# Optimization experiments

Measured on AMD Instinct MI355X. Metric: run time of the kernel, lower is better.

The kernel has to match this reference:

```python
import jax, jax.numpy as jnp
import numpy as np

N_NODES = 100000
N_REL = 4
N_EDGES = 160000  # per relation
IN_F, HID_F, OUT_F = 128, 128, 64


def hetero_layer(x, edges, W, b):
    """Sum over relations of GraphConv (norm='both'): D_in^-1/2 A_r D_out^-1/2 X W_r + b_r."""
    N = x.shape[0]
    out = jnp.zeros((N, W.shape[2]), dtype=x.dtype)
    for r in range(W.shape[0]):  # small fixed relation count
        src = edges[r, 0]
        dst = edges[r, 1]
        ones = jnp.ones(src.shape[0], dtype=x.dtype)
        deg_out = jnp.clip(jax.ops.segment_sum(ones, src, num_segments=N), 1.0)
        deg_in = jnp.clip(jax.ops.segment_sum(ones, dst, num_segments=N), 1.0)
        # scale src features, project (W first since in_feats >= out_feats), gather, scatter-sum
        h = (x * jax.lax.rsqrt(deg_out)[:, None]) @ W[r]
        agg = jax.ops.segment_sum(h[src], dst, num_segments=N)
        out = out + agg * jax.lax.rsqrt(deg_in)[:, None] + b[r]
    return out


def setup_inputs() -> dict:
    key = jax.random.key(0)
    ks = jax.random.split(key, 6)
    x = jax.random.normal(ks[0], (N_NODES, IN_F), dtype=jnp.float32)
    edges = jax.random.randint(ks[1], (N_REL, 2, N_EDGES), 0, N_NODES, dtype=jnp.int32)
    W1 = jax.random.normal(ks[2], (N_REL, IN_F, HID_F), dtype=jnp.float32) * 0.05
    b1 = jnp.zeros((N_REL, HID_F), dtype=jnp.float32)
    W2 = jax.random.normal(ks[3], (N_REL, HID_F, OUT_F), dtype=jnp.float32) * 0.05
    b2 = jnp.zeros((N_REL, OUT_F), dtype=jnp.float32)
    return {"x": x, "edges": edges, "W1": W1, "b1": b1, "W2": W2, "b2": b2}


def reference(x, edges, W1, b1, W2, b2):
    h = jax.nn.relu(hetero_layer(x, edges, W1, b1))
    return hetero_layer(h, edges, W2, b2)
```

## Files before the change

kernel.cpp:

```cpp
#include <hip/hip_runtime.h>
#include <cstddef>
#include <cstdint>

#define NN   100000
#define NR   4
#define NE   160000
#define SCAN_B 1024
#define GEMMB 512

typedef short bf16x8 __attribute__((ext_vector_type(8)));
typedef float f32x4  __attribute__((ext_vector_type(4)));

__device__ __forceinline__ unsigned short f2bf(float f) {
  union { float f; unsigned u; } v; v.f = f;
  unsigned r = v.u + 0x7fffu + ((v.u >> 16) & 1u);
  return (unsigned short)(r >> 16);
}
__device__ __forceinline__ float bf2f(unsigned short h) {
  union { unsigned u; float f; } v; v.u = ((unsigned)h) << 16;
  return v.f;
}

__device__ __forceinline__ void gll16(const unsigned short* g, unsigned short* l) {
  __builtin_amdgcn_global_load_lds(
      (const __attribute__((address_space(1))) void*)g,
      (__attribute__((address_space(3))) void*)l, 16, 0, 0);
}

#define A_ZERO 782
#define A_NBLK (A_ZERO + 6250 + 256 + 128 + 1)
__global__ __launch_bounds__(256) void phaseA_k(const float* __restrict__ x,
                                                const float* __restrict__ W1,
                                                const float* __restrict__ W2,
                                                const float* __restrict__ b1,
                                                const float* __restrict__ b2,
                                                int* __restrict__ cnt,
                                                unsigned short* __restrict__ xb,
                                                unsigned short* __restrict__ Wt1,
                                                unsigned short* __restrict__ Wt2,
                                                float* __restrict__ bs1,
                                                float* __restrict__ bs2) {
  const int bid = blockIdx.x;
  const int t = threadIdx.x;
  if (bid < A_ZERO) {
    const int i = bid * 256 + t;
    if (i < 2 * NR * NN / 4) ((int4*)cnt)[i] = make_int4(0, 0, 0, 0);
  } else if (bid < A_ZERO + 6250) {
    const int i = (bid - A_ZERO) * 256 + t;
    const float4 a = *(const float4*)&x[(size_t)i * 8];
    const float4 b = *(const float4*)&x[(size_t)i * 8 + 4];
    unsigned short o[8];
    o[0] = f2bf(a.x); o[1] = f2bf(a.y); o[2] = f2bf(a.z); o[3] = f2bf(a.w);
    o[4] = f2bf(b.x); o[5] = f2bf(b.y); o[6] = f2bf(b.z); o[7] = f2bf(b.w);
    *(bf16x8*)&xb[(size_t)i * 8] = *(bf16x8*)o;
  } else if (bid < A_ZERO + 6250 + 256) {
    const int i = (bid - A_ZERO - 6250) * 256 + t;
    const int r = i / (128 * 128);
    const int k = (i / 128) % 128;
    const int n = i % 128;
    Wt1[((size_t)r * 128 + n) * 128 + k] = f2bf(W1[i]);
  } else if (bid < A_ZERO + 6250 + 256 + 128) {
    const int i = (bid - A_ZERO - 6250 - 256) * 256 + t;
    const int r = i / (128 * 64);
    const int k = (i / 64) % 128;
    const int n = i % 64;
    Wt2[((size_t)r * 64 + n) * 128 + k] = f2bf(W2[i]);
  } else {
    if (t < 128) bs1[t] = b1[t] + b1[128 + t] + b1[256 + t] + b1[384 + t];
    if (t < 64)  bs2[t] = b2[t] + b2[64 + t] + b2[128 + t] + b2[192 + t];
  }
}

template <int NOUT>
__device__ __forceinline__ void gemm_core(const unsigned short* __restrict__ Xb,
                                          const unsigned short* __restrict__ Wtr,
                                          unsigned short* __restrict__ Hr,
                                          int vb, unsigned short (*Xl)[64 * 128]) {
  const int t = threadIdx.x;
  const int wid = t >> 6;
  const int lane = t & 63;
  const int lg = lane >> 4;
  const int lr = lane & 15;

  constexpr int NF = (NOUT == 128) ? 4 : 2;
  const int rbase = (wid & 1) * 32;
  const int cbase = (wid >> 1) * (NOUT / 2);

  bf16x8 bw[NF][4];
#pragma unroll
  for (int nf = 0; nf < NF; ++nf)
#pragma unroll
    for (int ks = 0; ks < 4; ++ks)
      bw[nf][ks] = *(const bf16x8*)&Wtr[(size_t)(cbase + nf * 16 + lr) * 128 + ks * 32 + lg * 8];

  auto stage = [&](int buf, int tile) {
    const int row0 = tile * 64;
#pragma unroll
    for (int i = 0; i < 4; ++i) {
      const int rl = wid * 16 + i * 4 + (lane >> 4);
      int gr = row0 + rl;
      if (gr >= NN) gr = NN - 1;
      const int q = (lane & 15) ^ (rl & 7);
      gll16(&Xb[(size_t)gr * 128 + q * 8], &Xl[buf][rl * 128 + (lane & 15) * 8]);
    }
  };

  const int ntiles = (NN + 63) / 64;
  int tile = vb;
  stage(0, tile);
  __syncthreads();
  int buf = 0;

  for (; tile < ntiles; tile += 128) {
    const int nxt = tile + 128;
    if (nxt < ntiles) stage(buf ^ 1, nxt);

    f32x4 acc[2][NF];
#pragma unroll
    for (int mf = 0; mf < 2; ++mf)
#pragma unroll
      for (int nf = 0; nf < NF; ++nf) acc[mf][nf] = (f32x4){0.f, 0.f, 0.f, 0.f};

#pragma unroll
    for (int ks = 0; ks < 4; ++ks) {
#pragma unroll
      for (int mf = 0; mf < 2; ++mf) {
        const int r = rbase + mf * 16 + lr;
        const bf16x8 a =
            *(const bf16x8*)&Xl[buf][r * 128 + (((ks * 4 + lg) ^ (lr & 7)) << 3)];
#pragma unroll
        for (int nf = 0; nf < NF; ++nf)
          acc[mf][nf] = __builtin_amdgcn_mfma_f32_16x16x32_bf16(a, bw[nf][ks], acc[mf][nf], 0, 0, 0);
      }
    }

    const int row0 = tile * 64;
#pragma unroll
    for (int mf = 0; mf < 2; ++mf) {
#pragma unroll
      for (int i = 0; i < 4; ++i) {
        const int row = row0 + rbase + mf * 16 + lg * 4 + i;
        if (row < NN) {
#pragma unroll
          for (int nf = 0; nf < NF; ++nf)
            Hr[(size_t)row * NOUT + cbase + nf * 16 + lr] = f2bf(acc[mf][nf][i]);
        }
      }
    }
    __syncthreads();
    buf ^= 1;
  }
}

__global__ __launch_bounds__(256, 2) void phaseB_k(const int* __restrict__ edges,
                                                   const unsigned short* __restrict__ xb,
                                                   const unsigned short* __restrict__ Wt1,
                                                   unsigned short* __restrict__ H,
                                                   int* __restrict__ cnt_out,
                                                   int* __restrict__ cnt_in) {
  __shared__ unsigned short Xl[2][64 * 128];
  const int bid = blockIdx.x;
  if (bid < GEMMB) {
    const int z = bid >> 7;
    gemm_core<128>(xb, Wt1 + (size_t)z * 128 * 128, H + (size_t)z * NN * 128, bid & 127, Xl);
    return;
  }
  const int idx = bid - GEMMB;
  const int r = idx / 625;
  const int e = (idx - r * 625) * 256 + threadIdx.x;
  const int s = edges[(size_t)r * 2 * NE + e];
  const int d = edges[(size_t)r * 2 * NE + NE + e];
  atomicAdd(&cnt_out[(size_t)r * NN + s], 1);
  atomicAdd(&cnt_in[(size_t)r * NN + d], 1);
}

template <int NOUT>
__global__ __launch_bounds__(256, 2) void gemm3_k(const unsigned short* __restrict__ Xb,
                                                  const unsigned short* __restrict__ Wt,
                                                  unsigned short* __restrict__ H) {
  __shared__ unsigned short Xl[2][64 * 128];
  const int z = blockIdx.z;
  gemm_core<NOUT>(Xb, Wt + (size_t)z * NOUT * 128, H + (size_t)z * NN * NOUT, blockIdx.x, Xl);
}

__global__ __launch_bounds__(256) void scan1_k(const int* __restrict__ cnt_in,
                                               int* __restrict__ excl,
                                               int* __restrict__ bsum) {
  const int b = blockIdx.x, t = threadIdx.x;
  const int base = b * SCAN_B;
  int v[4]; int tl = 0;
#pragma unroll
  for (int i = 0; i < 4; ++i) {
    const int idx = base + t * 4 + i;
    int c = 0;
    if (idx < NN) {
      c = cnt_in[idx] + cnt_in[NN + idx] + cnt_in[2 * NN + idx] + cnt_in[3 * NN + idx];
    }
    v[i] = c;
    tl += c;
  }
  __shared__ int sm[256];
  sm[t] = tl;
  __syncthreads();
  for (int off = 1; off < 256; off <<= 1) {
    const int x = (t >= off) ? sm[t - off] : 0;
    __syncthreads();
    sm[t] += x;
    __syncthreads();
  }
  const int incl = sm[t];
  int run = incl - tl;
#pragma unroll
  for (int i = 0; i < 4; ++i) {
    const int idx = base + t * 4 + i;
    if (idx < NN) excl[idx] = run;
    run += v[i];
  }
  if (t == 255) bsum[b] = incl;
}

__global__ __launch_bounds__(128) void scan2_k(int* __restrict__ bsum, int nb) {
  const int t = threadIdx.x;
  __shared__ int sm[128];
  const int v = (t < nb) ? bsum[t] : 0;
  sm[t] = v;
  __syncthreads();
  for (int off = 1; off < 128; off <<= 1) {
    const int x = (t >= off) ? sm[t - off] : 0;
    __syncthreads();
    sm[t] += x;
    __syncthreads();
  }
  if (t < nb) bsum[t] = sm[t] - v;
}

__global__ __launch_bounds__(256) void scan3rs_k(const int* __restrict__ cnt,
                                                 float* __restrict__ rs,
                                                 const int* __restrict__ bsum,
                                                 int* __restrict__ row_ptr,
                                                 int* __restrict__ cursor) {
  const int bid = blockIdx.x, t = threadIdx.x;
  if (bid < 3125) {
    const int i = bid * 256 + t;
    rs[i] = rsqrtf(fmaxf((float)cnt[i], 1.0f));
  } else {
    const int i = (bid - 3125) * 256 + t;
    if (i < NN) {
      const int v = cursor[i] + bsum[i / SCAN_B];
      row_ptr[i] = v;
      cursor[i] = v;
    }
    if (i == 0) row_ptr[NN] = NR * NE;
  }
}

__global__ __launch_bounds__(256) void fill_k(const int* __restrict__ edges,
                                              const float* __restrict__ rs_out,
                                              const float* __restrict__ rs_in,
                                              int* __restrict__ cursor,
                                              int2* __restrict__ csr) {
  const int r = blockIdx.y;
  const int e = blockIdx.x * 256 + threadIdx.x;
  if (e >= NE) return;
  const int s = edges[(size_t)r * 2 * NE + e];
  const int d = edges[(size_t)r * 2 * NE + NE + e];
  const int pos = atomicAdd(&cursor[d], 1);
  const float w = rs_in[(size_t)r * NN + d] * rs_out[(size_t)r * NN + s];
  csr[pos] = make_int2(r * NN + s, __float_as_int(w));
}

__global__ __launch_bounds__(256) void gather1_k(const unsigned short* __restrict__ H,
                                                 const int* __restrict__ row_ptr,
                                                 const int2* __restrict__ csr,
                                                 const float* __restrict__ bs1,
                                                 unsigned short* __restrict__ h1b) {
  const int node = blockIdx.x * 4 + (threadIdx.x >> 6);
  const int lane = threadIdx.x & 63;
  if (node >= NN) return;
  const int g  = lane >> 4;
  const int fl = lane & 15;

  float acc[8];
#pragma unroll
  for (int j = 0; j < 8; ++j) acc[j] = 0.f;

  const int beg = row_ptr[node];
  const int end = row_ptr[node + 1];
  for (int e = beg + g; e < end; e += 4) {
    const int2 p = csr[e];
    const float w = __int_as_float(p.y);
    const bf16x8 h = *(const bf16x8*)&H[(size_t)p.x * 128 + fl * 8];
#pragma unroll
    for (int j = 0; j < 8; ++j)
      acc[j] = fmaf(bf2f((unsigned short)h[j]), w, acc[j]);
  }
#pragma unroll
  for (int j = 0; j < 8; ++j) {
    acc[j] += __shfl_xor(acc[j], 16);
    acc[j] += __shfl_xor(acc[j], 32);
  }
  if (g == 0) {
    const float4 c0 = *(const float4*)&bs1[fl * 8];
    const float4 c1 = *(const float4*)&bs1[fl * 8 + 4];
    unsigned short o[8];
    o[0] = f2bf(fmaxf(acc[0] + c0.x, 0.f));
    o[1] = f2bf(fmaxf(acc[1] + c0.y, 0.f));
    o[2] = f2bf(fmaxf(acc[2] + c0.z, 0.f));
    o[3] = f2bf(fmaxf(acc[3] + c0.w, 0.f));
    o[4] = f2bf(fmaxf(acc[4] + c1.x, 0.f));
    o[5] = f2bf(fmaxf(acc[5] + c1.y, 0.f));
    o[6] = f2bf(fmaxf(acc[6] + c1.z, 0.f));
    o[7] = f2bf(fmaxf(acc[7] + c1.w, 0.f));
    *(bf16x8*)&h1b[(size_t)node * 128 + fl * 8] = *(bf16x8*)o;
  }
}

__global__ __launch_bounds__(256) void gather2_k(const unsigned short* __restrict__ H,
                                                 const int* __restrict__ row_ptr,
                                                 const int2* __restrict__ csr,
                                                 const float* __restrict__ bs2,
                                                 float* __restrict__ out) {
  const int node = blockIdx.x * 4 + (threadIdx.x >> 6);
  const int lane = threadIdx.x & 63;
  if (node >= NN) return;
  const int g  = lane >> 3;
  const int fl = lane & 7;

  float acc[8];
#pragma unroll
  for (int j = 0; j < 8; ++j) acc[j] = 0.f;

  const int beg = row_ptr[node];
  const int end = row_ptr[node + 1];
  for (int e = beg + g; e < end; e += 8) {
    const int2 p = csr[e];
    const float w = __int_as_float(p.y);
    const bf16x8 h = *(const bf16x8*)&H[(size_t)p.x * 64 + fl * 8];
#pragma unroll
    for (int j = 0; j < 8; ++j)
      acc[j] = fmaf(bf2f((unsigned short)h[j]), w, acc[j]);
  }
#pragma unroll
  for (int j = 0; j < 8; ++j) {
    acc[j] += __shfl_xor(acc[j], 8);
    acc[j] += __shfl_xor(acc[j], 16);
    acc[j] += __shfl_xor(acc[j], 32);
  }
  if (g == 0) {
    const float4 c0 = *(const float4*)&bs2[fl * 8];
    const float4 c1 = *(const float4*)&bs2[fl * 8 + 4];
    float4 o0, o1;
    o0.x = acc[0] + c0.x; o0.y = acc[1] + c0.y; o0.z = acc[2] + c0.z; o0.w = acc[3] + c0.w;
    o1.x = acc[4] + c1.x; o1.y = acc[5] + c1.y; o1.z = acc[6] + c1.z; o1.w = acc[7] + c1.w;
    *(float4*)&out[(size_t)node * 64 + fl * 8]     = o0;
    *(float4*)&out[(size_t)node * 64 + fl * 8 + 4] = o1;
  }
}

extern "C" void kernel_launch(void* const* d_in, const int* in_sizes, int n_in,
                              void* d_out, int out_size, void* d_ws, size_t ws_size,
                              hipStream_t stream) {
  const float* x     = (const float*)d_in[0];
  const int*   edges = (const int*)d_in[1];
  const float* W1    = (const float*)d_in[2];
  const float* b1    = (const float*)d_in[3];
  const float* W2    = (const float*)d_in[4];
  const float* b2    = (const float*)d_in[5];
  float* out = (float*)d_out;

  unsigned short* xb   = (unsigned short*)d_ws;
  unsigned short* h1b  = xb;
  unsigned short* Hbuf = xb + (size_t)NN * 128;
  unsigned short* Wt1  = Hbuf + (size_t)NR * NN * 128;
  unsigned short* Wt2  = Wt1 + (size_t)NR * 128 * 128;
  float* rs_out = (float*)(Wt2 + (size_t)NR * 64 * 128);
  float* rs_in  = rs_out + (size_t)NR * NN;
  int* cnt_out  = (int*)(rs_in + (size_t)NR * NN);
  int* cnt_in   = cnt_out + (size_t)NR * NN;
  int* row_ptr  = cnt_in + (size_t)NR * NN;
  int* cursor   = row_ptr + (NN + 1);
  int* bsum     = cursor + NN;
  float* bs1    = (float*)(bsum + 128);
  float* bs2    = bs1 + 128;
  int2* csr     = (int2*)(bs2 + 64);

  const int nb = (NN + SCAN_B - 1) / SCAN_B;

  phaseA_k<<<A_NBLK, 256, 0, stream>>>(x, W1, W2, b1, b2, cnt_out, xb, Wt1, Wt2, bs1, bs2);
  phaseB_k<<<GEMMB + 2500, 256, 0, stream>>>(edges, xb, Wt1, Hbuf, cnt_out, cnt_in);
  scan1_k<<<nb, 256, 0, stream>>>(cnt_in, cursor , bsum);
  scan2_k<<<1, 128, 0, stream>>>(bsum, nb);
  scan3rs_k<<<3125 + (NN + 255) / 256, 256, 0, stream>>>(cnt_out, rs_out, bsum, row_ptr, cursor);
  fill_k<<<dim3((NE + 255) / 256, NR), 256, 0, stream>>>(edges, rs_out, rs_in, cursor, csr);
  gather1_k<<<(NN + 3) / 4, 256, 0, stream>>>(Hbuf, row_ptr, csr, bs1, h1b);
  gemm3_k<64><<<dim3(128, 1, NR), 256, 0, stream>>>(h1b, Wt2, Hbuf);
  gather2_k<<<(NN + 3) / 4, 256, 0, stream>>>(Hbuf, row_ptr, csr, bs2, out);
}
```

Measured before the change: 214.9 us.

## Reschedule phases: fuse degree counting into prep, pair GEMM with CSR fill, widen gathers

The zeroing of the degree counters becomes a memset, and edge degree counting moves into the first prep kernel. The layer-1 GEMM now shares a launch with the CSR fill instead of the counting step, so GEMM blocks overlap with the fill. The second-layer GEMM processes two relations per block so each staged input tile is reused for both, and both gather kernels give each lane 16 features, spreading more edges per node across lanes. Together these aim to cut launches and redundant input loads, at the cost of more registers per lane in the gathers and an extra memset call.

```diff
diff --git a/kernel.cpp b/kernel.cpp
--- a/kernel.cpp
+++ b/kernel.cpp
@@ -27,14 +27,15 @@
       (__attribute__((address_space(3))) void*)l, 16, 0, 0);
 }
 
-#define A_ZERO 782
-#define A_NBLK (A_ZERO + 6250 + 256 + 128 + 1)
-__global__ __launch_bounds__(256) void phaseA_k(const float* __restrict__ x,
+#define P1_NBLK 9135
+__global__ __launch_bounds__(256) void phase1_k(const int* __restrict__ edges,
+                                                const float* __restrict__ x,
                                                 const float* __restrict__ W1,
                                                 const float* __restrict__ W2,
                                                 const float* __restrict__ b1,
                                                 const float* __restrict__ b2,
-                                                int* __restrict__ cnt,
+                                                int* __restrict__ cnt_out,
+                                                int* __restrict__ cnt_in,
                                                 unsigned short* __restrict__ xb,
                                                 unsigned short* __restrict__ Wt1,
                                                 unsigned short* __restrict__ Wt2,
@@ -42,25 +43,29 @@
                                                 float* __restrict__ bs2) {
   const int bid = blockIdx.x;
   const int t = threadIdx.x;
-  if (bid < A_ZERO) {
-    const int i = bid * 256 + t;
-    if (i < 2 * NR * NN / 4) ((int4*)cnt)[i] = make_int4(0, 0, 0, 0);
-  } else if (bid < A_ZERO + 6250) {
-    const int i = (bid - A_ZERO) * 256 + t;
+  if (bid < 2500) {
+    const int r = bid / 625;
+    const int e = (bid - r * 625) * 256 + t;
+    const int s = edges[(size_t)r * 2 * NE + e];
+    const int d = edges[(size_t)r * 2 * NE + NE + e];
+    atomicAdd(&cnt_out[(size_t)r * NN + s], 1);
+    atomicAdd(&cnt_in[(size_t)r * NN + d], 1);
+  } else if (bid < 8750) {
+    const int i = (bid - 2500) * 256 + t;
     const float4 a = *(const float4*)&x[(size_t)i * 8];
     const float4 b = *(const float4*)&x[(size_t)i * 8 + 4];
     unsigned short o[8];
     o[0] = f2bf(a.x); o[1] = f2bf(a.y); o[2] = f2bf(a.z); o[3] = f2bf(a.w);
     o[4] = f2bf(b.x); o[5] = f2bf(b.y); o[6] = f2bf(b.z); o[7] = f2bf(b.w);
     *(bf16x8*)&xb[(size_t)i * 8] = *(bf16x8*)o;
-  } else if (bid < A_ZERO + 6250 + 256) {
-    const int i = (bid - A_ZERO - 6250) * 256 + t;
+  } else if (bid < 9006) {
+    const int i = (bid - 8750) * 256 + t;
     const int r = i / (128 * 128);
     const int k = (i / 128) % 128;
     const int n = i % 128;
     Wt1[((size_t)r * 128 + n) * 128 + k] = f2bf(W1[i]);
-  } else if (bid < A_ZERO + 6250 + 256 + 128) {
-    const int i = (bid - A_ZERO - 6250 - 256) * 256 + t;
+  } else if (bid < 9134) {
+    const int i = (bid - 9006) * 256 + t;
     const int r = i / (128 * 64);
     const int k = (i / 64) % 128;
     const int n = i % 64;
@@ -69,118 +74,6 @@
     if (t < 128) bs1[t] = b1[t] + b1[128 + t] + b1[256 + t] + b1[384 + t];
     if (t < 64)  bs2[t] = b2[t] + b2[64 + t] + b2[128 + t] + b2[192 + t];
   }
-}
-
-template <int NOUT>
-__device__ __forceinline__ void gemm_core(const unsigned short* __restrict__ Xb,
-                                          const unsigned short* __restrict__ Wtr,
-                                          unsigned short* __restrict__ Hr,
-                                          int vb, unsigned short (*Xl)[64 * 128]) {
-  const int t = threadIdx.x;
-  const int wid = t >> 6;
-  const int lane = t & 63;
-  const int lg = lane >> 4;
-  const int lr = lane & 15;
-
-  constexpr int NF = (NOUT == 128) ? 4 : 2;
-  const int rbase = (wid & 1) * 32;
-  const int cbase = (wid >> 1) * (NOUT / 2);
-
-  bf16x8 bw[NF][4];
-#pragma unroll
-  for (int nf = 0; nf < NF; ++nf)
-#pragma unroll
-    for (int ks = 0; ks < 4; ++ks)
-      bw[nf][ks] = *(const bf16x8*)&Wtr[(size_t)(cbase + nf * 16 + lr) * 128 + ks * 32 + lg * 8];
-
-  auto stage = [&](int buf, int tile) {
-    const int row0 = tile * 64;
-#pragma unroll
-    for (int i = 0; i < 4; ++i) {
-      const int rl = wid * 16 + i * 4 + (lane >> 4);
-      int gr = row0 + rl;
-      if (gr >= NN) gr = NN - 1;
-      const int q = (lane & 15) ^ (rl & 7);
-      gll16(&Xb[(size_t)gr * 128 + q * 8], &Xl[buf][rl * 128 + (lane & 15) * 8]);
-    }
-  };
-
-  const int ntiles = (NN + 63) / 64;
-  int tile = vb;
-  stage(0, tile);
-  __syncthreads();
-  int buf = 0;
-
-  for (; tile < ntiles; tile += 128) {
-    const int nxt = tile + 128;
-    if (nxt < ntiles) stage(buf ^ 1, nxt);
-
-    f32x4 acc[2][NF];
-#pragma unroll
-    for (int mf = 0; mf < 2; ++mf)
-#pragma unroll
-      for (int nf = 0; nf < NF; ++nf) acc[mf][nf] = (f32x4){0.f, 0.f, 0.f, 0.f};
-
-#pragma unroll
-    for (int ks = 0; ks < 4; ++ks) {
-#pragma unroll
-      for (int mf = 0; mf < 2; ++mf) {
-        const int r = rbase + mf * 16 + lr;
-        const bf16x8 a =
-            *(const bf16x8*)&Xl[buf][r * 128 + (((ks * 4 + lg) ^ (lr & 7)) << 3)];
-#pragma unroll
-        for (int nf = 0; nf < NF; ++nf)
-          acc[mf][nf] = __builtin_amdgcn_mfma_f32_16x16x32_bf16(a, bw[nf][ks], acc[mf][nf], 0, 0, 0);
-      }
-    }
-
-    const int row0 = tile * 64;
-#pragma unroll
-    for (int mf = 0; mf < 2; ++mf) {
-#pragma unroll
-      for (int i = 0; i < 4; ++i) {
-        const int row = row0 + rbase + mf * 16 + lg * 4 + i;
-        if (row < NN) {
-#pragma unroll
-          for (int nf = 0; nf < NF; ++nf)
-            Hr[(size_t)row * NOUT + cbase + nf * 16 + lr] = f2bf(acc[mf][nf][i]);
-        }
-      }
-    }
-    __syncthreads();
-    buf ^= 1;
-  }
-}
-
-__global__ __launch_bounds__(256, 2) void phaseB_k(const int* __restrict__ edges,
-                                                   const unsigned short* __restrict__ xb,
-                                                   const unsigned short* __restrict__ Wt1,
-                                                   unsigned short* __restrict__ H,
-                                                   int* __restrict__ cnt_out,
-                                                   int* __restrict__ cnt_in) {
-  __shared__ unsigned short Xl[2][64 * 128];
-  const int bid = blockIdx.x;
-  if (bid < GEMMB) {
-    const int z = bid >> 7;
-    gemm_core<128>(xb, Wt1 + (size_t)z * 128 * 128, H + (size_t)z * NN * 128, bid & 127, Xl);
-    return;
-  }
-  const int idx = bid - GEMMB;
-  const int r = idx / 625;
-  const int e = (idx - r * 625) * 256 + threadIdx.x;
-  const int s = edges[(size_t)r * 2 * NE + e];
-  const int d = edges[(size_t)r * 2 * NE + NE + e];
-  atomicAdd(&cnt_out[(size_t)r * NN + s], 1);
-  atomicAdd(&cnt_in[(size_t)r * NN + d], 1);
-}
-
-template <int NOUT>
-__global__ __launch_bounds__(256, 2) void gemm3_k(const unsigned short* __restrict__ Xb,
-                                                  const unsigned short* __restrict__ Wt,
-                                                  unsigned short* __restrict__ H) {
-  __shared__ unsigned short Xl[2][64 * 128];
-  const int z = blockIdx.z;
-  gemm_core<NOUT>(Xb, Wt + (size_t)z * NOUT * 128, H + (size_t)z * NN * NOUT, blockIdx.x, Xl);
 }
 
 __global__ __launch_bounds__(256) void scan1_k(const int* __restrict__ cnt_in,
@@ -254,19 +147,203 @@
   }
 }
 
-__global__ __launch_bounds__(256) void fill_k(const int* __restrict__ edges,
-                                              const float* __restrict__ rs_out,
-                                              const float* __restrict__ rs_in,
-                                              int* __restrict__ cursor,
-                                              int2* __restrict__ csr) {
-  const int r = blockIdx.y;
-  const int e = blockIdx.x * 256 + threadIdx.x;
-  if (e >= NE) return;
+template <int NOUT>
+__device__ __forceinline__ void gemm_core(const unsigned short* __restrict__ Xb,
+                                          const unsigned short* __restrict__ Wtr,
+                                          unsigned short* __restrict__ Hr,
+                                          int vb, unsigned short (*Xl)[64 * 128]) {
+  const int t = threadIdx.x;
+  const int wid = t >> 6;
+  const int lane = t & 63;
+  const int lg = lane >> 4;
+  const int lr = lane & 15;
+
+  constexpr int NF = (NOUT == 128) ? 4 : 2;
+  const int rbase = (wid & 1) * 32;
+  const int cbase = (wid >> 1) * (NOUT / 2);
+
+  bf16x8 bw[NF][4];
+#pragma unroll
+  for (int nf = 0; nf < NF; ++nf)
+#pragma unroll
+    for (int ks = 0; ks < 4; ++ks)
+      bw[nf][ks] = *(const bf16x8*)&Wtr[(size_t)(cbase + nf * 16 + lr) * 128 + ks * 32 + lg * 8];
+
+  auto stage = [&](int buf, int tile) {
+    const int row0 = tile * 64;
+#pragma unroll
+    for (int i = 0; i < 4; ++i) {
+      const int rl = wid * 16 + i * 4 + (lane >> 4);
+      int gr = row0 + rl;
+      if (gr >= NN) gr = NN - 1;
+      const int q = (lane & 15) ^ (rl & 7);
+      gll16(&Xb[(size_t)gr * 128 + q * 8], &Xl[buf][rl * 128 + (lane & 15) * 8]);
+    }
+  };
+
+  const int ntiles = (NN + 63) / 64;
+  int tile = vb;
+  stage(0, tile);
+  __syncthreads();
+  int buf = 0;
+
+  for (; tile < ntiles; tile += 128) {
+    const int nxt = tile + 128;
+    if (nxt < ntiles) stage(buf ^ 1, nxt);
+
+    f32x4 acc[2][NF];
+#pragma unroll
+    for (int mf = 0; mf < 2; ++mf)
+#pragma unroll
+      for (int nf = 0; nf < NF; ++nf) acc[mf][nf] = (f32x4){0.f, 0.f, 0.f, 0.f};
+
+#pragma unroll
+    for (int ks = 0; ks < 4; ++ks) {
+#pragma unroll
+      for (int mf = 0; mf < 2; ++mf) {
+        const int r = rbase + mf * 16 + lr;
+        const bf16x8 a =
+            *(const bf16x8*)&Xl[buf][r * 128 + (((ks * 4 + lg) ^ (lr & 7)) << 3)];
+#pragma unroll
+        for (int nf = 0; nf < NF; ++nf)
+          acc[mf][nf] = __builtin_amdgcn_mfma_f32_16x16x32_bf16(a, bw[nf][ks], acc[mf][nf], 0, 0, 0);
+      }
+    }
+
+    const int row0 = tile * 64;
+#pragma unroll
+    for (int mf = 0; mf < 2; ++mf) {
+#pragma unroll
+      for (int i = 0; i < 4; ++i) {
+        const int row = row0 + rbase + mf * 16 + lg * 4 + i;
+        if (row < NN) {
+#pragma unroll
+          for (int nf = 0; nf < NF; ++nf)
+            Hr[(size_t)row * NOUT + cbase + nf * 16 + lr] = f2bf(acc[mf][nf][i]);
+        }
+      }
+    }
+    __syncthreads();
+    buf ^= 1;
+  }
+}
+
+__global__ __launch_bounds__(256, 2) void phaseC_k(const int* __restrict__ edges,
+                                                   const unsigned short* __restrict__ xb,
+                                                   const unsigned short* __restrict__ Wt1,
+                                                   unsigned short* __restrict__ H,
+                                                   const float* __restrict__ rs_out,
+                                                   const float* __restrict__ rs_in,
+                                                   int* __restrict__ cursor,
+                                                   int2* __restrict__ csr) {
+  __shared__ unsigned short Xl[2][64 * 128];
+  const int bid = blockIdx.x;
+  if (bid < GEMMB) {
+    const int z = bid >> 7;
+    gemm_core<128>(xb, Wt1 + (size_t)z * 128 * 128, H + (size_t)z * NN * 128, bid & 127, Xl);
+    return;
+  }
+  const int vb = bid - GEMMB;
+  const int r = vb / 625;
+  const int e = (vb - r * 625) * 256 + threadIdx.x;
   const int s = edges[(size_t)r * 2 * NE + e];
   const int d = edges[(size_t)r * 2 * NE + NE + e];
   const int pos = atomicAdd(&cursor[d], 1);
   const float w = rs_in[(size_t)r * NN + d] * rs_out[(size_t)r * NN + s];
   csr[pos] = make_int2(r * NN + s, __float_as_int(w));
+}
+
+__global__ __launch_bounds__(256, 2) void gemm_dual_k(const unsigned short* __restrict__ Xb,
+                                                      const unsigned short* __restrict__ Wt,
+                                                      unsigned short* __restrict__ H) {
+  __shared__ unsigned short Xl[2][64 * 128];
+  const int zp = blockIdx.z;
+  const unsigned short* W0 = Wt + (size_t)(2 * zp) * 64 * 128;
+  const unsigned short* W1 = Wt + (size_t)(2 * zp + 1) * 64 * 128;
+  unsigned short* H0 = H + (size_t)(2 * zp) * NN * 64;
+  unsigned short* H1 = H + (size_t)(2 * zp + 1) * NN * 64;
+
+  const int t = threadIdx.x;
+  const int wid = t >> 6;
+  const int lane = t & 63;
+  const int lg = lane >> 4;
+  const int lr = lane & 15;
+
+  const int rbase = (wid & 1) * 32;
+  const int cbase = (wid >> 1) * 32;
+
+  bf16x8 bw[2][2][4];
+#pragma unroll
+  for (int nf = 0; nf < 2; ++nf)
+#pragma unroll
+    for (int ks = 0; ks < 4; ++ks) {
+      bw[0][nf][ks] = *(const bf16x8*)&W0[(size_t)(cbase + nf * 16 + lr) * 128 + ks * 32 + lg * 8];
+      bw[1][nf][ks] = *(const bf16x8*)&W1[(size_t)(cbase + nf * 16 + lr) * 128 + ks * 32 + lg * 8];
+    }
+
+  auto stage = [&](int buf, int tile) {
+    const int row0 = tile * 64;
+#pragma unroll
+    for (int i = 0; i < 4; ++i) {
+      const int rl = wid * 16 + i * 4 + (lane >> 4);
+      int gr = row0 + rl;
+      if (gr >= NN) gr = NN - 1;
+      const int q = (lane & 15) ^ (rl & 7);
+      gll16(&Xb[(size_t)gr * 128 + q * 8], &Xl[buf][rl * 128 + (lane & 15) * 8]);
+    }
+  };
+
+  const int ntiles = (NN + 63) / 64;
+  int tile = blockIdx.x;
+  stage(0, tile);
+  __syncthreads();
+  int buf = 0;
+
+  for (; tile < ntiles; tile += 128) {
+    const int nxt = tile + 128;
+    if (nxt < ntiles) stage(buf ^ 1, nxt);
+
+    f32x4 acc[2][2][2];
+#pragma unroll
+    for (int mf = 0; mf < 2; ++mf)
+#pragma unroll
+      for (int rel = 0; rel < 2; ++rel)
+#pragma unroll
+        for (int nf = 0; nf < 2; ++nf) acc[mf][rel][nf] = (f32x4){0.f, 0.f, 0.f, 0.f};
+
+#pragma unroll
+    for (int ks = 0; ks < 4; ++ks) {
+#pragma unroll
+      for (int mf = 0; mf < 2; ++mf) {
+        const int r = rbase + mf * 16 + lr;
+        const bf16x8 a =
+            *(const bf16x8*)&Xl[buf][r * 128 + (((ks * 4 + lg) ^ (lr & 7)) << 3)];
+#pragma unroll
+        for (int rel = 0; rel < 2; ++rel)
+#pragma unroll
+          for (int nf = 0; nf < 2; ++nf)
+            acc[mf][rel][nf] = __builtin_amdgcn_mfma_f32_16x16x32_bf16(a, bw[rel][nf][ks], acc[mf][rel][nf], 0, 0, 0);
+      }
+    }
+
+    const int row0 = tile * 64;
+#pragma unroll
+    for (int mf = 0; mf < 2; ++mf) {
+#pragma unroll
+      for (int i = 0; i < 4; ++i) {
+        const int row = row0 + rbase + mf * 16 + lg * 4 + i;
+        if (row < NN) {
+#pragma unroll
+          for (int nf = 0; nf < 2; ++nf) {
+            H0[(size_t)row * 64 + cbase + nf * 16 + lr] = f2bf(acc[mf][0][nf][i]);
+            H1[(size_t)row * 64 + cbase + nf * 16 + lr] = f2bf(acc[mf][1][nf][i]);
+          }
+        }
+      }
+    }
+    __syncthreads();
+    buf ^= 1;
+  }
 }
 
 __global__ __launch_bounds__(256) void gather1_k(const unsigned short* __restrict__ H,
@@ -277,41 +354,39 @@
   const int node = blockIdx.x * 4 + (threadIdx.x >> 6);
   const int lane = threadIdx.x & 63;
   if (node >= NN) return;
-  const int g  = lane >> 4;
-  const int fl = lane & 15;
-
-  float acc[8];
-#pragma unroll
-  for (int j = 0; j < 8; ++j) acc[j] = 0.f;
+  const int g  = lane >> 3;
+  const int fl = lane & 7;
+
+  float acc[16];
+#pragma unroll
+  for (int j = 0; j < 16; ++j) acc[j] = 0.f;
 
   const int beg = row_ptr[node];
   const int end = row_ptr[node + 1];
-  for (int e = beg + g; e < end; e += 4) {
+  for (int e = beg + g; e < end; e += 8) {
     const int2 p = csr[e];
     const float w = __int_as_float(p.y);
-    const bf16x8 h = *(const bf16x8*)&H[(size_t)p.x * 128 + fl * 8];
-#pragma unroll
-    for (int j = 0; j < 8; ++j)
-      acc[j] = fmaf(bf2f((unsigned short)h[j]), w, acc[j]);
-  }
-#pragma unroll
-  for (int j = 0; j < 8; ++j) {
+    const bf16x8 h0 = *(const bf16x8*)&H[(size_t)p.x * 128 + fl * 16];
+    const bf16x8 h1 = *(const bf16x8*)&H[(size_t)p.x * 128 + fl * 16 + 8];
+#pragma unroll
+    for (int j = 0; j < 8; ++j) {
+      acc[j]     = fmaf(bf2f((unsigned short)h0[j]), w, acc[j]);
+      acc[8 + j] = fmaf(bf2f((unsigned short)h1[j]), w, acc[8 + j]);
+    }
+  }
+#pragma unroll
+  for (int j = 0; j < 16; ++j) {
+    acc[j] += __shfl_xor(acc[j], 8);
     acc[j] += __shfl_xor(acc[j], 16);
     acc[j] += __shfl_xor(acc[j], 32);
   }
   if (g == 0) {
-    const float4 c0 = *(const float4*)&bs1[fl * 8];
-    const float4 c1 = *(const float4*)&bs1[fl * 8 + 4];
-    unsigned short o[8];
-    o[0] = f2bf(fmaxf(acc[0] + c0.x, 0.f));
-    o[1] = f2bf(fmaxf(acc[1] + c0.y, 0.f));
-    o[2] = f2bf(fmaxf(acc[2] + c0.z, 0.f));
-    o[3] = f2bf(fmaxf(acc[3] + c0.w, 0.f));
-    o[4] = f2bf(fmaxf(acc[4] + c1.x, 0.f));
-    o[5] = f2bf(fmaxf(acc[5] + c1.y, 0.f));
-    o[6] = f2bf(fmaxf(acc[6] + c1.z, 0.f));
-    o[7] = f2bf(fmaxf(acc[7] + c1.w, 0.f));
-    *(bf16x8*)&h1b[(size_t)node * 128 + fl * 8] = *(bf16x8*)o;
+    unsigned short o[16];
+#pragma unroll
+    for (int j = 0; j < 16; ++j)
+      o[j] = f2bf(fmaxf(acc[j] + bs1[fl * 16 + j], 0.f));
+    *(bf16x8*)&h1b[(size_t)node * 128 + fl * 16]     = *(bf16x8*)&o[0];
+    *(bf16x8*)&h1b[(size_t)node * 128 + fl * 16 + 8] = *(bf16x8*)&o[8];
   }
 }
 
@@ -323,37 +398,41 @@
   const int node = blockIdx.x * 4 + (threadIdx.x >> 6);
   const int lane = threadIdx.x & 63;
   if (node >= NN) return;
-  const int g  = lane >> 3;
-  const int fl = lane & 7;
-
-  float acc[8];
-#pragma unroll
-  for (int j = 0; j < 8; ++j) acc[j] = 0.f;
+  const int g  = lane >> 2;
+  const int fl = lane & 3;
+
+  float acc[16];
+#pragma unroll
+  for (int j = 0; j < 16; ++j) acc[j] = 0.f;
 
   const int beg = row_ptr[node];
   const int end = row_ptr[node + 1];
-  for (int e = beg + g; e < end; e += 8) {
+  for (int e = beg + g; e < end; e += 16) {
     const int2 p = csr[e];
     const float w = __int_as_float(p.y);
-    const bf16x8 h = *(const bf16x8*)&H[(size_t)p.x * 64 + fl * 8];
-#pragma unroll
-    for (int j = 0; j < 8; ++j)
-      acc[j] = fmaf(bf2f((unsigned short)h[j]), w, acc[j]);
-  }
-#pragma unroll
-  for (int j = 0; j < 8; ++j) {
+    const bf16x8 h0 = *(const bf16x8*)&H[(size_t)p.x * 64 + fl * 16];
+    const bf16x8 h1 = *(const bf16x8*)&H[(size_t)p.x * 64 + fl * 16 + 8];
+#pragma unroll
+    for (int j = 0; j < 8; ++j) {
+      acc[j]     = fmaf(bf2f((unsigned short)h0[j]), w, acc[j]);
+      acc[8 + j] = fmaf(bf2f((unsigned short)h1[j]), w, acc[8 + j]);
+    }
+  }
+#pragma unroll
+  for (int j = 0; j < 16; ++j) {
+    acc[j] += __shfl_xor(acc[j], 4);
     acc[j] += __shfl_xor(acc[j], 8);
     acc[j] += __shfl_xor(acc[j], 16);
     acc[j] += __shfl_xor(acc[j], 32);
   }
   if (g == 0) {
-    const float4 c0 = *(const float4*)&bs2[fl * 8];
-    const float4 c1 = *(const float4*)&bs2[fl * 8 + 4];
-    float4 o0, o1;
-    o0.x = acc[0] + c0.x; o0.y = acc[1] + c0.y; o0.z = acc[2] + c0.z; o0.w = acc[3] + c0.w;
-    o1.x = acc[4] + c1.x; o1.y = acc[5] + c1.y; o1.z = acc[6] + c1.z; o1.w = acc[7] + c1.w;
-    *(float4*)&out[(size_t)node * 64 + fl * 8]     = o0;
-    *(float4*)&out[(size_t)node * 64 + fl * 8 + 4] = o1;
+    float o[16];
+#pragma unroll
+    for (int j = 0; j < 16; ++j) o[j] = acc[j] + bs2[fl * 16 + j];
+    *(float4*)&out[(size_t)node * 64 + fl * 16]      = *(float4*)&o[0];
+    *(float4*)&out[(size_t)node * 64 + fl * 16 + 4]  = *(float4*)&o[4];
+    *(float4*)&out[(size_t)node * 64 + fl * 16 + 8]  = *(float4*)&o[8];
+    *(float4*)&out[(size_t)node * 64 + fl * 16 + 12] = *(float4*)&o[12];
   }
 }
 
@@ -386,13 +465,14 @@
 
   const int nb = (NN + SCAN_B - 1) / SCAN_B;
 
-  phaseA_k<<<A_NBLK, 256, 0, stream>>>(x, W1, W2, b1, b2, cnt_out, xb, Wt1, Wt2, bs1, bs2);
-  phaseB_k<<<GEMMB + 2500, 256, 0, stream>>>(edges, xb, Wt1, Hbuf, cnt_out, cnt_in);
+  hipMemsetAsync(cnt_out, 0, (size_t)2 * NR * NN * sizeof(int), stream);
+  phase1_k<<<P1_NBLK, 256, 0, stream>>>(edges, x, W1, W2, b1, b2,
+                                        cnt_out, cnt_in, xb, Wt1, Wt2, bs1, bs2);
   scan1_k<<<nb, 256, 0, stream>>>(cnt_in, cursor , bsum);
   scan2_k<<<1, 128, 0, stream>>>(bsum, nb);
   scan3rs_k<<<3125 + (NN + 255) / 256, 256, 0, stream>>>(cnt_out, rs_out, bsum, row_ptr, cursor);
-  fill_k<<<dim3((NE + 255) / 256, NR), 256, 0, stream>>>(edges, rs_out, rs_in, cursor, csr);
+  phaseC_k<<<GEMMB + 2500, 256, 0, stream>>>(edges, xb, Wt1, Hbuf, rs_out, rs_in, cursor, csr);
   gather1_k<<<(NN + 3) / 4, 256, 0, stream>>>(Hbuf, row_ptr, csr, bs1, h1b);
-  gemm3_k<64><<<dim3(128, 1, NR), 256, 0, stream>>>(h1b, Wt2, Hbuf);
+  gemm_dual_k<<<dim3(128, 1, 2), 256, 0, stream>>>(h1b, Wt2, Hbuf);
   gather2_k<<<(NN + 3) / 4, 256, 0, stream>>>(Hbuf, row_ptr, csr, bs2, out);
 }
```

Result: slower. 267.4 us (+24.4%).
